# Performance work log

Hardware: AMD Instinct MI355X
Metric: run time of the kernel (lower is better)

## Reference

```python
import jax, jax.numpy as jnp
import numpy as np

KH, KW = 2, 2

def setup_inputs() -> dict:
    key = jax.random.key(0)
    k1, k2 = jax.random.split(key)
    x = jax.random.normal(k1, (64, 32, 32, 32), dtype=jnp.float32)
    # logits = log(rand) in torch; emulate with log of uniform to keep same distribution family
    logits = jnp.log(jax.random.uniform(k2, (32, 32, 32, 32), dtype=jnp.float32, minval=1e-6, maxval=1.0))
    return {"x": x, "logits": logits}


def reference(x, logits):
    # SumLayer: log_softmax over in_channels (dim=1), broadcast add, logsumexp over in
    log_w = jax.nn.log_softmax(logits, axis=1)            # [O, I, H, W]
    # x: [N, I, H, W] -> [N, 1, I, H, W]; log_w -> [1, O, I, H, W]
    y = jax.scipy.special.logsumexp(x[:, None] + log_w[None], axis=2)  # [N, O, H, W]
    # ProdConv: grouped conv with ones kernel, stride (KH,KW) == non-overlapping sum-pool
    N, C, H, W = y.shape
    y = y.reshape(N, C, H // KH, KH, W // KW, KW).sum(axis=(3, 5))     # [N, O, H/KH, W/KW]
    return y
```

## Files before the change

### kernel.cpp

```cpp
#include <hip/hip_runtime.h>

namespace {
constexpr int IC = 32;
constexpr int OC = 32;
constexpr int HW = 1024;
constexpr int H2 = 16, W2 = 16;

typedef _Float16 half2v __attribute__((ext_vector_type(2)));

#if defined(__has_builtin)
#if __has_builtin(__builtin_amdgcn_fdot2)
#define HAVE_FDOT2 1
#endif
#endif

__device__ __forceinline__ float dot2acc(half2v a, half2v b, float c) {
#ifdef HAVE_FDOT2
    return __builtin_amdgcn_fdot2(a, b, c, false);
#else
    return fmaf((float)a.x, (float)b.x, fmaf((float)a.y, (float)b.y, c));
#endif
}

__device__ __forceinline__ half2v u2h(unsigned int u) {
    union { unsigned int u; half2v h; } x; x.u = u; return x.h;
}

__device__ __forceinline__ half2v pk2(float a, float b) {
    union { decltype(__builtin_amdgcn_cvt_pkrtz(0.f, 0.f)) p; half2v h; } x;
    x.p = __builtin_amdgcn_cvt_pkrtz(a, b);
    return x.h;
}
}

__global__ __launch_bounds__(512, 4) void sumprod_fused(
    const float* __restrict__ x, const float* __restrict__ logits,
    float* __restrict__ out)
{
    __shared__ half2v exl[8 * 64 * 16];
    __shared__ half2v ewl[8 * 64 * 16];
    __shared__ float  wsl[8 * 64];

    const int tid  = threadIdx.x;
    const int lane = tid & 63;
    const int w    = tid >> 6;
    const int bid  = blockIdx.x;
    const int s    = bid & 15;
    const int tt   = bid >> 4;
    const int n0   = (tt & 7) * 8;
    const int o0   = (tt >> 3) * 8;

    const int kk    = (tid >> 4) & 3;
    const int p4    = tid & 15;
    const int spoff = (2 * s + (p4 >> 3)) * 32 + (p4 & 7) * 4;

    const float* gx = x      + (size_t)(n0 + w) * IC * HW + spoff;
    const float* gw = logits + (size_t)(o0 + w) * IC * HW + spoff;

    auto stage = [&](half2v* buf, const float4& va, const float4& vb, int ip) {
        const float* pa = reinterpret_cast<const float*>(&va);
        const float* pb = reinterpret_cast<const float*>(&vb);
        #pragma unroll
        for (int j = 0; j < 4; ++j) {
            const int p    = (p4 >> 3) * 32 + (p4 & 7) * 4 + j;
            const int slot = (ip >> 2) ^ (((p >> 1) ^ (p >> 3)) & 3);
            buf[(w * 64 + p) * 16 + slot * 4 + (ip & 3)] =
                pk2(__expf(pa[j]), __expf(pb[j]));
        }
    };

    #pragma unroll
    for (int g = 0; g < 4; ++g) {
        const int ip = g * 4 + kk;
        const float4 va = *reinterpret_cast<const float4*>(&gw[(2 * ip) * HW]);
        const float4 vb = *reinterpret_cast<const float4*>(&gw[(2 * ip + 1) * HW]);
        stage(ewl, va, vb, ip);
    }
    #pragma unroll
    for (int g = 0; g < 2; ++g) {
        const int ip = g * 4 + kk;
        const float4 va = *reinterpret_cast<const float4*>(&gx[(2 * ip) * HW]);
        const float4 vb = *reinterpret_cast<const float4*>(&gx[(2 * ip + 1) * HW]);
        stage(exl, va, vb, ip);
    }
    __syncthreads();

    float4 pva[2], pvb[2];
    #pragma unroll
    for (int g = 0; g < 2; ++g) {
        const int ip = (g + 2) * 4 + kk;
        pva[g] = *reinterpret_cast<const float4*>(&gx[(2 * ip) * HW]);
        pvb[g] = *reinterpret_cast<const float4*>(&gx[(2 * ip + 1) * HW]);
    }

    const int swl = ((lane >> 1) ^ (lane >> 3)) & 3;

    {
        float ds = 0.f;
        const half2v one2 = {(_Float16)1.f, (_Float16)1.f};
        #pragma unroll
        for (int gg = 0; gg < 4; ++gg) {
            const uint4 B = *reinterpret_cast<const uint4*>(
                &ewl[(w * 64 + lane) * 16 + ((gg ^ swl) * 4)]);
            ds = dot2acc(u2h(B.x), one2, ds);
            ds = dot2acc(u2h(B.y), one2, ds);
            ds = dot2acc(u2h(B.z), one2, ds);
            ds = dot2acc(u2h(B.w), one2, ds);
        }
        wsl[w * 64 + lane] = ds;
    }

    const int nw = (w & 1) * 4;
    const int ow = (w >> 1) * 2;
    float acc[4][2] = {};

#define D2(AA, BB, K, J) acc[K][J] = dot2acc(u2h(AA), u2h(BB), acc[K][J])
#define QUAD(A_, K_)                                                          \
    D2(A_.x, B0.x, K_, 0); D2(A_.y, B0.y, K_, 0);                             \
    D2(A_.z, B0.z, K_, 0); D2(A_.w, B0.w, K_, 0);                             \
    D2(A_.x, B1.x, K_, 1); D2(A_.y, B1.y, K_, 1);                             \
    D2(A_.z, B1.z, K_, 1); D2(A_.w, B1.w, K_, 1)
#define COMPUTE_GG(GG) {                                                      \
    const int off = ((GG) ^ swl) * 4;                                         \
    const uint4 A0 = *reinterpret_cast<const uint4*>(&exl[((nw + 0) * 64 + lane) * 16 + off]); \
    const uint4 A1 = *reinterpret_cast<const uint4*>(&exl[((nw + 1) * 64 + lane) * 16 + off]); \
    const uint4 A2 = *reinterpret_cast<const uint4*>(&exl[((nw + 2) * 64 + lane) * 16 + off]); \
    const uint4 A3 = *reinterpret_cast<const uint4*>(&exl[((nw + 3) * 64 + lane) * 16 + off]); \
    const uint4 B0 = *reinterpret_cast<const uint4*>(&ewl[((ow + 0) * 64 + lane) * 16 + off]); \
    const uint4 B1 = *reinterpret_cast<const uint4*>(&ewl[((ow + 1) * 64 + lane) * 16 + off]); \
    QUAD(A0, 0); QUAD(A1, 1); QUAD(A2, 2); QUAD(A3, 3); }

    COMPUTE_GG(0);
    COMPUTE_GG(1);

    #pragma unroll
    for (int g = 0; g < 2; ++g) {
        const int ip = (g + 2) * 4 + kk;
        stage(exl, pva[g], pvb[g], ip);
    }
    __syncthreads();

    COMPUTE_GG(2);
    COMPUTE_GG(3);

#undef COMPUTE_GG
#undef QUAD
#undef D2

    const float lw0 = __logf(wsl[(ow + 0) * 64 + lane]);
    const float lw1 = __logf(wsl[(ow + 1) * 64 + lane]);

    #pragma unroll
    for (int k = 0; k < 4; ++k) {
        #pragma unroll
        for (int j = 0; j < 2; ++j) {
            float v = __logf(acc[k][j]) - (j ? lw1 : lw0);
            v += __shfl_xor(v, 1);
            v += __shfl_xor(v, 32);
            if ((lane & 33) == 0) {
                const int w2 = (lane >> 1) & 15;
                out[((n0 + nw + k) * OC + (o0 + ow + j)) * (H2 * W2) + s * W2 + w2] = v;
            }
        }
    }
}

extern "C" void kernel_launch(void* const* d_in, const int* in_sizes, int n_in,
                              void* d_out, int out_size, void* d_ws, size_t ws_size,
                              hipStream_t stream) {
    const float* x      = (const float*)d_in[0];
    const float* logits = (const float*)d_in[1];
    float* out = (float*)d_out;
    hipLaunchKernelGGL(sumprod_fused, dim3(512), dim3(512), 0, stream,
                       x, logits, out);
}
```

Measured before the change: 12.68 us.

## Stage all x channels up front, compute denominators in-register, reduce via products

Loads and stages all 32 x input channels before a single barrier, which removes the split prefetch and the second __syncthreads. Each wave now computes the softmax denominators for its own output channels directly from LDS, so the wsl shared array and its cross-wave dependency go away. The 2x2 pooling reduction now multiplies values across lanes and takes one log per output rather than a log per lane, which cuts transcendental work. The risks are the loss of load/compute overlap from the old prefetch, and possible float overflow or underflow in the product of four exp-sums.

```diff
diff --git a/kernel.cpp b/kernel.cpp
--- a/kernel.cpp
+++ b/kernel.cpp
@@ -39,7 +39,6 @@
 {
     __shared__ half2v exl[8 * 64 * 16];
     __shared__ half2v ewl[8 * 64 * 16];
-    __shared__ float  wsl[8 * 64];
 
     const int tid  = threadIdx.x;
     const int lane = tid & 63;
@@ -77,7 +76,7 @@
         stage(ewl, va, vb, ip);
     }
     #pragma unroll
-    for (int g = 0; g < 2; ++g) {
+    for (int g = 0; g < 4; ++g) {
         const int ip = g * 4 + kk;
         const float4 va = *reinterpret_cast<const float4*>(&gx[(2 * ip) * HW]);
         const float4 vb = *reinterpret_cast<const float4*>(&gx[(2 * ip + 1) * HW]);
@@ -85,33 +84,27 @@
     }
     __syncthreads();
 
-    float4 pva[2], pvb[2];
+    const int swl = ((lane >> 1) ^ (lane >> 3)) & 3;
+    const int nw = (w & 1) * 4;
+    const int ow = (w >> 1) * 2;
+
+    const half2v one2 = {(_Float16)1.f, (_Float16)1.f};
+    float den[2];
     #pragma unroll
-    for (int g = 0; g < 2; ++g) {
-        const int ip = (g + 2) * 4 + kk;
-        pva[g] = *reinterpret_cast<const float4*>(&gx[(2 * ip) * HW]);
-        pvb[g] = *reinterpret_cast<const float4*>(&gx[(2 * ip + 1) * HW]);
-    }
-
-    const int swl = ((lane >> 1) ^ (lane >> 3)) & 3;
-
-    {
+    for (int j = 0; j < 2; ++j) {
         float ds = 0.f;
-        const half2v one2 = {(_Float16)1.f, (_Float16)1.f};
+        const half2v* rb = &ewl[((ow + j) * 64 + lane) * 16];
         #pragma unroll
         for (int gg = 0; gg < 4; ++gg) {
-            const uint4 B = *reinterpret_cast<const uint4*>(
-                &ewl[(w * 64 + lane) * 16 + ((gg ^ swl) * 4)]);
+            const uint4 B = *reinterpret_cast<const uint4*>(rb + ((gg ^ swl) * 4));
             ds = dot2acc(u2h(B.x), one2, ds);
             ds = dot2acc(u2h(B.y), one2, ds);
             ds = dot2acc(u2h(B.z), one2, ds);
             ds = dot2acc(u2h(B.w), one2, ds);
         }
-        wsl[w * 64 + lane] = ds;
+        den[j] = ds;
     }
 
-    const int nw = (w & 1) * 4;
-    const int ow = (w >> 1) * 2;
     float acc[4][2] = {};
 
 #define D2(AA, BB, K, J) acc[K][J] = dot2acc(u2h(AA), u2h(BB), acc[K][J])
@@ -132,14 +125,6 @@
 
     COMPUTE_GG(0);
     COMPUTE_GG(1);
-
-    #pragma unroll
-    for (int g = 0; g < 2; ++g) {
-        const int ip = (g + 2) * 4 + kk;
-        stage(exl, pva[g], pvb[g], ip);
-    }
-    __syncthreads();
-
     COMPUTE_GG(2);
     COMPUTE_GG(3);
 
@@ -147,19 +132,22 @@
 #undef QUAD
 #undef D2
 
-    const float lw0 = __logf(wsl[(ow + 0) * 64 + lane]);
-    const float lw1 = __logf(wsl[(ow + 1) * 64 + lane]);
+    float dp0 = den[0];
+    dp0 *= __shfl_xor(dp0, 1);  dp0 *= __shfl_xor(dp0, 32);
+    float dp1 = den[1];
+    dp1 *= __shfl_xor(dp1, 1);  dp1 *= __shfl_xor(dp1, 32);
 
     #pragma unroll
     for (int k = 0; k < 4; ++k) {
         #pragma unroll
         for (int j = 0; j < 2; ++j) {
-            float v = __logf(acc[k][j]) - (j ? lw1 : lw0);
-            v += __shfl_xor(v, 1);
-            v += __shfl_xor(v, 32);
+            float v = acc[k][j];
+            v *= __shfl_xor(v, 1);
+            v *= __shfl_xor(v, 32);
             if ((lane & 33) == 0) {
                 const int w2 = (lane >> 1) & 15;
-                out[((n0 + nw + k) * OC + (o0 + ow + j)) * (H2 * W2) + s * W2 + w2] = v;
+                out[((n0 + nw + k) * OC + (o0 + ow + j)) * (H2 * W2) + s * W2 + w2] =
+                    __logf(v) - __logf(j ? dp1 : dp0);
             }
         }
     }
```

Measured after the change: 13.45 us. 6.1% more time.
